# Kernel optimization log

Hardware: AMD Instinct MI355X
Metric: run time of the kernel (lower is better)

## Reference

```python
import jax, jax.numpy as jnp
import numpy as np

N, M, D = 32768, 1024, 128
TAU = 1.0  # gumbel-softmax temperature (forward default)


def setup_inputs() -> dict:
    key = jax.random.key(0)
    k1, k2, k3 = jax.random.split(key, 3)
    x = jax.random.normal(k1, (N, D), dtype=jnp.float32)
    embedding = jax.random.normal(k2, (M, D), dtype=jnp.float32)
    # torch: log_var_q_scalar initialized to log(10.0)
    log_var_q_scalar = jnp.full((1,), np.log(10.0), dtype=jnp.float32)
    # uniform noise for gumbel-softmax (replaces torch.rand_like)
    u = jax.random.uniform(k3, (N, M), dtype=jnp.float32)
    return {"x": x, "embedding": embedding,
            "log_var_q_scalar": log_var_q_scalar, "u": u}


def reference(x, embedding, log_var_q_scalar, u):
    # gaussian_1: a single scalar precision shared by all tokens/dims, so the
    # precision-weighted squared distance factorizes; expand ||x-e||^2 via a
    # GEMM instead of materializing the (N, M, D) broadcast tensor.
    precision = jnp.exp(-log_var_q_scalar)[0]                 # scalar
    x2 = jnp.sum(x * x, axis=-1, keepdims=True)               # (N, 1)
    e2 = jnp.sum(embedding * embedding, axis=-1)              # (M,)
    xe = x @ embedding.T                                      # (N, M)
    distances = 0.5 * precision * (x2 - 2.0 * xe + e2)        # (N, M)

    indices = jnp.argmin(distances, axis=-1)                  # (N,) int
    logits = -distances

    # gumbel-softmax (soft)
    eps = jnp.finfo(logits.dtype).eps
    gumbels = -jnp.log(-jnp.log(jnp.clip(u, eps, 1.0 - eps)))
    encodings = jax.nn.softmax((logits + gumbels) / TAU, axis=-1)  # (N, M)
    quantized = encodings @ embedding                              # (N, D)

    log_probs = jax.nn.log_softmax(logits, axis=-1)
    probs = jnp.exp(log_probs)
    # torch.mean over a 0-d result == the scalar itself
    loss = 0.5 * precision * jnp.sum((x - quantized) ** 2) \
           + jnp.sum(probs * log_probs)

    one_hot = jax.nn.one_hot(indices, embedding.shape[0], dtype=jnp.float32)
    avg_probs = jnp.mean(one_hot, axis=0)
    perplexity = jnp.exp(-jnp.sum(avg_probs * jnp.log(avg_probs + 1e-10)))
    return quantized, indices, loss, perplexity
```

## Files before the change

kernel.cpp:

```cpp
#include <hip/hip_runtime.h>
#include <math.h>

#define N_TOK 32768
#define M_EMB 1024
#define D_DIM 128

#define WS_EH  0
#define WS_EL  262144
#define WS_PVG 524288
#define WS_E2  1048576
#define WS_CNT (WS_E2 + 4096)
#define WS_SS  (WS_CNT + 4096)
#define WS_ENT (WS_SS + 4)
#define WS_DONE (WS_ENT + 4)

typedef float  f32x4  __attribute__((ext_vector_type(4)));
typedef short  s16x8  __attribute__((ext_vector_type(8)));
typedef short  s16x4  __attribute__((ext_vector_type(4)));
typedef __bf16 bf16x8 __attribute__((ext_vector_type(8)));

__device__ __forceinline__ ushort f2bf(float f) {
    unsigned x = __float_as_uint(f);
    unsigned r = (x + 0x7fffu + ((x >> 16) & 1u)) >> 16;
    return (ushort)r;
}
__device__ __forceinline__ float bf2f(ushort h) {
    return __uint_as_float(((unsigned)h) << 16);
}
__device__ __forceinline__ f32x4 mfma_k32(s16x8 a, s16x8 b, f32x4 c) {
    return __builtin_amdgcn_mfma_f32_16x16x32_bf16(
        __builtin_bit_cast(bf16x8, a), __builtin_bit_cast(bf16x8, b), c, 0, 0, 0);
}
__device__ __forceinline__ f32x4 mfma_k16(s16x4 a, s16x4 b, f32x4 c) {
#if __has_builtin(__builtin_amdgcn_mfma_f32_16x16x16bf16_1k)
    return __builtin_amdgcn_mfma_f32_16x16x16bf16_1k(a, b, c, 0, 0, 0);
#else
    asm("v_mfma_f32_16x16x16_bf16 %0, %1, %2, %0" : "+v"(c) : "v"(a), "v"(b));
    return c;
#endif
}
__device__ __forceinline__ void gl_lds16(const void* g, void* l) {
    __builtin_amdgcn_global_load_lds(
        (const __attribute__((address_space(1))) unsigned int*)g,
        (__attribute__((address_space(3))) unsigned int*)l, 16, 0, 0);
}

__global__ void k_prep(const float* __restrict__ emb, char* ws) {
    __shared__ ushort th_s[16][128];
    __shared__ ushort tl_s[16][128];
    if (blockIdx.x == 0) {
        int* cnt = (int*)(ws + WS_CNT);
        for (int i = threadIdx.x; i < M_EMB; i += 256) cnt[i] = 0;
        if (threadIdx.x == 0) {
            *(float*)(ws + WS_SS) = 0.f;
            *(float*)(ws + WS_ENT) = 0.f;
            *(int*)(ws + WS_DONE) = 0;
        }
    }
    ushort* eh = (ushort*)(ws + WS_EH);
    ushort* el = (ushort*)(ws + WS_EL);
    ushort* pvg = (ushort*)(ws + WS_PVG);
    float* e2 = (float*)(ws + WS_E2);
    const int m0 = blockIdx.x * 16;
    const int t = threadIdx.x;
    #pragma unroll
    for (int ii = 0; ii < 8; ii++) {
        int idx = t + ii * 256;
        int mi = idx >> 7, k = idx & 127;
        float v = emb[(size_t)(m0 + mi) * D_DIM + k];
        ushort hi = f2bf(v);
        ushort lo = f2bf(v - bf2f(hi));
        eh[(size_t)(m0 + mi) * D_DIM + k] = hi;
        el[(size_t)(m0 + mi) * D_DIM + k] = lo;
        th_s[mi][k] = hi;
        tl_s[mi][k] = lo;
    }
    __syncthreads();
    {
        const int d = t >> 1;
        const int gl2 = t & 1;
        #pragma unroll
        for (int gg = 0; gg < 2; gg++) {
            const int gl = gl2 * 2 + gg;
            s16x8 vv;
            #pragma unroll
            for (int kk = 0; kk < 4; kk++) {
                vv[kk]     = (short)th_s[gl * 4 + kk][d];
                vv[4 + kk] = (short)tl_s[gl * 4 + kk][d];
            }
            *(s16x8*)(pvg + (size_t)d * 2048 + ((m0 >> 2) + gl) * 8) = vv;
        }
    }
    if (t < 16) {
        float s = 0.f;
        const float* er = emb + (size_t)(m0 + t) * D_DIM;
        #pragma unroll 4
        for (int k = 0; k < 128; k++) s += er[k] * er[k];
        e2[m0 + t] = s;
    }
}

__global__ __launch_bounds__(256, 2) void k_main(
    const float* __restrict__ x, const float* __restrict__ emb,
    const float* __restrict__ lvq, const float* __restrict__ u,
    float* __restrict__ out, char* __restrict__ ws)
{
    __shared__ __align__(16) ushort qkh[2][32 * 128];
    __shared__ __align__(16) ushort qkl[2][32 * 128];
    __shared__ __align__(16) ushort pvt[2][128 * 64];
    __shared__ int last_flag;
    __shared__ float fin[4];

    const int t = threadIdx.x;
    const int w = t >> 6;
    const int lane = t & 63;
    const int l15 = lane & 15;
    const int h = lane >> 4;
    const int n0w = blockIdx.x * 64 + w * 16;

    const float* e2g = (const float*)(ws + WS_E2);
    int* cnt = (int*)(ws + WS_CNT);
    float* ws_ss = (float*)(ws + WS_SS);
    float* ws_ent = (float*)(ws + WS_ENT);
    const char* EHb = (const char*)(ws + WS_EH);
    const char* ELb = (const char*)(ws + WS_EL);
    const char* PVGb = (const char*)(ws + WS_PVG);

    const float prec = expf(-lvq[0]);
    const float hp = 0.5f * prec;

    int offA[8];
    if (w < 2) {
        #pragma unroll
        for (int c = 0; c < 8; c++) {
            const int s = c * 1024 + lane * 16;
            offA[c] = s ^ (((s >> 8) & 7) << 4);
        }
    } else {
        #pragma unroll
        for (int c = 0; c < 8; c++) {
            const int s = ((w - 2) * 8 + c) * 1024 + lane * 16;
            const int d = s >> 7;
            offA[c] = d * 4096 + ((s ^ ((d & 7) << 4)) & 127);
        }
    }

    s16x8 xh[4], xl[4];
    {
        const float* xr = x + (size_t)(n0w + l15) * D_DIM;
        #pragma unroll
        for (int ks = 0; ks < 4; ks++) {
            const int k0 = ks * 32 + h * 8;
            float4 v0 = *(const float4*)(xr + k0);
            float4 v1 = *(const float4*)(xr + k0 + 4);
            float vv[8] = {v0.x, v0.y, v0.z, v0.w, v1.x, v1.y, v1.z, v1.w};
            s16x8 hi8, lo8;
            #pragma unroll
            for (int j = 0; j < 8; j++) {
                ushort hi = f2bf(vv[j]);
                hi8[j] = (short)hi;
                lo8[j] = (short)f2bf(vv[j] - bf2f(hi));
            }
            xh[ks] = hi8;
            xl[ks] = lo8;
        }
    }

    const f32x4 zz = {0.f, 0.f, 0.f, 0.f};
    f32x4 qacc[8];
    #pragma unroll
    for (int dt = 0; dt < 8; dt++) qacc[dt] = zz;

    float S = 0.f, T = 0.f, Sg = 0.f;
    float bv1 = -INFINITY, bv2 = -INFINITY;
    int bi1 = M_EMB, bi2 = M_EMB;

    const float* urow = u + (size_t)(n0w + l15) * M_EMB;
    const float EPS = 1.1920929e-07f, OME = 0.99999988f;

    #define STAGE(MB, B)                                                      \
        do {                                                                  \
            if (w == 0) {                                                     \
                const char* src_ = EHb + (size_t)(MB) * 256;                  \
                _Pragma("unroll")                                             \
                for (int c_ = 0; c_ < 8; c_++)                                \
                    gl_lds16(src_ + offA[c_], &qkh[B][c_ * 512]);             \
            } else if (w == 1) {                                              \
                const char* src_ = ELb + (size_t)(MB) * 256;                  \
                _Pragma("unroll")                                             \
                for (int c_ = 0; c_ < 8; c_++)                                \
                    gl_lds16(src_ + offA[c_], &qkl[B][c_ * 512]);             \
            } else {                                                          \
                const char* src_ = PVGb + (size_t)(MB) * 4;                   \
                _Pragma("unroll")                                             \
                for (int c_ = 0; c_ < 8; c_++)                                \
                    gl_lds16(src_ + offA[c_],                                 \
                             &pvt[B][((w - 2) * 8 + c_) * 512]);              \
            }                                                                 \
        } while (0)

    STAGE(0, 0);
    __syncthreads();

    int cur = 0;
    const int Mq = (l15 & 7) << 4;

    #pragma unroll 1
    for (int mc = 0; mc < 32; mc++) {
        const int mb = mc * 32;
        float4 uvv[2];
        #pragma unroll
        for (int t2 = 0; t2 < 2; t2++)
            uvv[t2] = *(const float4*)(urow + mb + t2 * 16 + h * 4);
        if (mc < 31) {
            if (cur) STAGE(mb + 32, 0); else STAGE(mb + 32, 1);
        }

        #pragma unroll
        for (int t2 = 0; t2 < 2; t2++) {
            const int msub = mb + t2 * 16;
            const int r = t2 * 16 + l15;
            const char* qhB = (const char*)qkh[cur] + r * 256;
            const char* qlB = (const char*)qkl[cur] + r * 256;
            f32x4 aa = zz, ab = zz, ac = zz;
            #pragma unroll
            for (int ks = 0; ks < 4; ks++) {
                const int cb = (h * 16 + ks * 64) ^ Mq;
                const s16x8 ah = *(const s16x8*)(qhB + cb);
                const s16x8 al = *(const s16x8*)(qlB + cb);
                aa = mfma_k32(ah, xh[ks], aa);
                ab = mfma_k32(al, xh[ks], ab);
                ac = mfma_k32(ah, xl[ks], ac);
            }
            const float4 e2v = *(const float4*)(e2g + msub + h * 4);
            const float uu[4] = {uvv[t2].x, uvv[t2].y, uvv[t2].z, uvv[t2].w};
            const float ee[4] = {e2v.x, e2v.y, e2v.z, e2v.w};
            ushort pb[4];
            #pragma unroll
            for (int j = 0; j < 4; j++) {
                const int m = msub + h * 4 + j;
                const float v = prec * (aa[j] + ab[j] + ac[j]) - hp * ee[j];
                if (v > bv1) {
                    bv2 = bv1; bi2 = bi1;
                    bv1 = v; bi1 = m;
                } else if (v > bv2) {
                    bv2 = v; bi2 = m;
                }
                const float e = __expf(v);
                S += e; T += e * v;
                const float uc = fminf(fmaxf(uu[j], EPS), OME);
                const float d1 = 1.0f - uc;
                const float Lser = d1 * (1.0f + d1 * (0.5f + d1 * (0.33333334f + d1 * 0.25f)));
                const float Lnat = -__logf(uc);
                const float L = (d1 < 0.03125f) ? Lser : Lnat;
                const float pt = e * __builtin_amdgcn_rcpf(L);
                Sg += pt;
                pb[j] = f2bf(pt);
            }
            s16x4 pa;
            pa[0] = (short)pb[0]; pa[1] = (short)pb[1];
            pa[2] = (short)pb[2]; pa[3] = (short)pb[3];
            const char* pvB = (const char*)pvt[cur]
                            + ((l15 * 128 + (t2 * 4 + h) * 16) ^ Mq);
            #pragma unroll
            for (int dt = 0; dt < 8; dt++) {
                const s16x8 pv2 = *(const s16x8*)(pvB + dt * 2048);
                const s16x4 bh = __builtin_shufflevector(pv2, pv2, 0, 1, 2, 3);
                const s16x4 bl = __builtin_shufflevector(pv2, pv2, 4, 5, 6, 7);
                qacc[dt] = mfma_k16(pa, bh, qacc[dt]);
                qacc[dt] = mfma_k16(pa, bl, qacc[dt]);
            }
        }
        __syncthreads();
        cur ^= 1;
    }
    #undef STAGE

    #pragma unroll
    for (int off = 16; off <= 32; off <<= 1) {
        S += __shfl_xor(S, off);
        T += __shfl_xor(T, off);
        Sg += __shfl_xor(Sg, off);
        const float ov1 = __shfl_xor(bv1, off); const int oi1 = __shfl_xor(bi1, off);
        const float ov2 = __shfl_xor(bv2, off); const int oi2 = __shfl_xor(bi2, off);
        if (ov1 > bv1 || (ov1 == bv1 && oi1 < bi1)) {
            if (bv1 > ov2 || (bv1 == ov2 && bi1 < oi2)) { bv2 = bv1; bi2 = bi1; }
            else { bv2 = ov2; bi2 = oi2; }
            bv1 = ov1; bi1 = oi1;
        } else if (ov1 > bv2 || (ov1 == bv2 && oi1 < bi2)) {
            bv2 = ov1; bi2 = oi1;
        }
    }
    float inv[4];
    #pragma unroll
    for (int j = 0; j < 4; j++)
        inv[j] = 1.0f / __shfl(Sg, 4 * h + j);

    {
        float ent = T / S - __logf(S);
        #pragma unroll
        for (int off = 1; off <= 8; off <<= 1) ent += __shfl_xor(ent, off);
        if (lane == 0) atomicAdd(ws_ent, ent);
    }

    {
        const float* xr = x + (size_t)(n0w + l15) * D_DIM + h * 32;
        const float* ea = emb + (size_t)bi1 * D_DIM + h * 32;
        const float* eb = emb + (size_t)bi2 * D_DIM + h * 32;
        float s1 = 0.f, s2 = 0.f;
        #pragma unroll
        for (int i = 0; i < 8; i++) {
            const float4 xv = ((const float4*)xr)[i];
            const float4 av = ((const float4*)ea)[i];
            const float4 bb = ((const float4*)eb)[i];
            s1 += xv.x * av.x + xv.y * av.y + xv.z * av.z + xv.w * av.w;
            s2 += xv.x * bb.x + xv.y * bb.y + xv.z * bb.z + xv.w * bb.w;
        }
        #pragma unroll
        for (int off = 16; off <= 32; off <<= 1) {
            s1 += __shfl_xor(s1, off);
            s2 += __shfl_xor(s2, off);
        }
        const float g1 = prec * s1 - hp * e2g[bi1];
        const float g2 = prec * s2 - hp * e2g[bi2];
        const int win = (g2 > g1 || (g2 == g1 && bi2 < bi1)) ? bi2 : bi1;
        if (lane < 16) {
            out[(size_t)N_TOK * D_DIM + n0w + lane] = (float)win;
            atomicAdd(&cnt[win], 1);
        }
    }

    float ssl = 0.f;
    #pragma unroll
    for (int dt = 0; dt < 8; dt++) {
        #pragma unroll
        for (int j = 0; j < 4; j++) {
            const int n = n0w + 4 * h + j;
            const int d = dt * 16 + l15;
            const float q = qacc[dt][j] * inv[j];
            out[(size_t)n * D_DIM + d] = q;
            const float df = x[(size_t)n * D_DIM + d] - q;
            ssl += df * df;
        }
    }
    #pragma unroll
    for (int off = 1; off <= 32; off <<= 1) ssl += __shfl_xor(ssl, off);
    if (lane == 0) atomicAdd(ws_ss, ssl);

    __syncthreads();
    if (t == 0) {
        const int prev = __hip_atomic_fetch_add((int*)(ws + WS_DONE), 1,
                            __ATOMIC_ACQ_REL, __HIP_MEMORY_SCOPE_AGENT);
        last_flag = (prev == (int)gridDim.x - 1);
    }
    __syncthreads();
    if (last_flag) {
        float s = 0.f;
        for (int i = t; i < M_EMB; i += 256) {
            const int c = __hip_atomic_load(&cnt[i], __ATOMIC_RELAXED,
                                            __HIP_MEMORY_SCOPE_AGENT);
            const float avg = (float)c * (1.f / N_TOK);
            s += avg * logf(avg + 1e-10f);
        }
        #pragma unroll
        for (int off = 32; off >= 1; off >>= 1) s += __shfl_down(s, off);
        if ((t & 63) == 0) fin[t >> 6] = s;
        __syncthreads();
        if (t == 0) {
            const float tot = fin[0] + fin[1] + fin[2] + fin[3];
            const float perp = expf(-tot);
            const float ssv = __hip_atomic_load(ws_ss, __ATOMIC_RELAXED,
                                                __HIP_MEMORY_SCOPE_AGENT);
            const float env = __hip_atomic_load(ws_ent, __ATOMIC_RELAXED,
                                                __HIP_MEMORY_SCOPE_AGENT);
            out[(size_t)N_TOK * D_DIM + N_TOK] = hp * ssv + env;
            out[(size_t)N_TOK * D_DIM + N_TOK + 1] = perp;
        }
    }
}

extern "C" void kernel_launch(void* const* d_in, const int* in_sizes, int n_in,
                              void* d_out, int out_size, void* d_ws, size_t ws_size,
                              hipStream_t stream) {
    const float* x   = (const float*)d_in[0];
    const float* emb = (const float*)d_in[1];
    const float* lvq = (const float*)d_in[2];
    const float* u   = (const float*)d_in[3];
    float* out = (float*)d_out;
    char* ws = (char*)d_ws;
    k_prep<<<dim3(M_EMB / 16), dim3(256), 0, stream>>>(emb, ws);
    k_main<<<dim3(N_TOK / 64), dim3(256), 0, stream>>>(x, emb, lvq, u, out, ws);
}
```

Baseline: 334.8 us.

## Split codebook range across wave pairs with 512-thread blocks and cross-wave merge

Each 64-token block now launches 512 threads, and every pair of waves shares 16 tokens. One wave of the pair handles the first half of the codebook and the other the second half. Each half-set of four waves stages its own tiles into its own LDS buffer. Softmax sums, top-2 argmin candidates and the quantized accumulators are merged through shared memory at the end. The aim is more waves per CU and a shorter serial loop per wave, at the cost of losing the double-buffered prefetch (now two barriers per step) and of extra merge traffic.

```diff
diff --git a/kernel.cpp b/kernel.cpp
--- a/kernel.cpp
+++ b/kernel.cpp
@@ -100,23 +100,26 @@
     }
 }
 
-__global__ __launch_bounds__(256, 2) void k_main(
+__global__ __launch_bounds__(512, 4) void k_main(
     const float* __restrict__ x, const float* __restrict__ emb,
     const float* __restrict__ lvq, const float* __restrict__ u,
     float* __restrict__ out, char* __restrict__ ws)
 {
-    __shared__ __align__(16) ushort qkh[2][32 * 128];
-    __shared__ __align__(16) ushort qkl[2][32 * 128];
-    __shared__ __align__(16) ushort pvt[2][128 * 64];
-    __shared__ int last_flag;
-    __shared__ float fin[4];
+    __shared__ __align__(16) ushort qkh2[2][32 * 128];
+    __shared__ __align__(16) ushort qkl2[2][32 * 128];
+    __shared__ __align__(16) ushort pvt2[2][128 * 64];
+    float* sf = (float*)pvt2;
 
     const int t = threadIdx.x;
     const int w = t >> 6;
     const int lane = t & 63;
     const int l15 = lane & 15;
     const int h = lane >> 4;
-    const int n0w = blockIdx.x * 64 + w * 16;
+    const int p = w >> 1;
+    const int q = w & 1;
+    const int rw = w & 3;
+    const int sset = w >> 2;
+    const int n0p = blockIdx.x * 64 + p * 16;
 
     const float* e2g = (const float*)(ws + WS_E2);
     int* cnt = (int*)(ws + WS_CNT);
@@ -130,24 +133,24 @@
     const float hp = 0.5f * prec;
 
     int offA[8];
-    if (w < 2) {
+    if (rw < 2) {
         #pragma unroll
         for (int c = 0; c < 8; c++) {
-            const int s = c * 1024 + lane * 16;
-            offA[c] = s ^ (((s >> 8) & 7) << 4);
+            const int s_ = c * 1024 + lane * 16;
+            offA[c] = s_ ^ (((s_ >> 8) & 7) << 4);
         }
     } else {
         #pragma unroll
         for (int c = 0; c < 8; c++) {
-            const int s = ((w - 2) * 8 + c) * 1024 + lane * 16;
-            const int d = s >> 7;
-            offA[c] = d * 4096 + ((s ^ ((d & 7) << 4)) & 127);
+            const int s_ = ((rw - 2) * 8 + c) * 1024 + lane * 16;
+            const int d_ = s_ >> 7;
+            offA[c] = d_ * 4096 + ((s_ ^ ((d_ & 7) << 4)) & 127);
         }
     }
 
     s16x8 xh[4], xl[4];
     {
-        const float* xr = x + (size_t)(n0w + l15) * D_DIM;
+        const float* xr = x + (size_t)(n0p + l15) * D_DIM;
         #pragma unroll
         for (int ks = 0; ks < 4; ks++) {
             const int k0 = ks * 32 + h * 8;
@@ -175,53 +178,51 @@
     float bv1 = -INFINITY, bv2 = -INFINITY;
     int bi1 = M_EMB, bi2 = M_EMB;
 
-    const float* urow = u + (size_t)(n0w + l15) * M_EMB;
+    const float* urow = u + (size_t)(n0p + l15) * M_EMB;
     const float EPS = 1.1920929e-07f, OME = 0.99999988f;
 
-    #define STAGE(MB, B)                                                      \
+    #define STAGE(S_)                                                         \
         do {                                                                  \
-            if (w == 0) {                                                     \
-                const char* src_ = EHb + (size_t)(MB) * 256;                  \
+            const int MB_ = ((sset << 4) + (S_)) << 5;                        \
+            if (rw == 0) {                                                    \
+                const char* src_ = EHb + (size_t)MB_ * 256;                   \
                 _Pragma("unroll")                                             \
                 for (int c_ = 0; c_ < 8; c_++)                                \
-                    gl_lds16(src_ + offA[c_], &qkh[B][c_ * 512]);             \
-            } else if (w == 1) {                                              \
-                const char* src_ = ELb + (size_t)(MB) * 256;                  \
+                    gl_lds16(src_ + offA[c_], &qkh2[sset][c_ * 512]);         \
+            } else if (rw == 1) {                                             \
+                const char* src_ = ELb + (size_t)MB_ * 256;                   \
                 _Pragma("unroll")                                             \
                 for (int c_ = 0; c_ < 8; c_++)                                \
-                    gl_lds16(src_ + offA[c_], &qkl[B][c_ * 512]);             \
+                    gl_lds16(src_ + offA[c_], &qkl2[sset][c_ * 512]);         \
             } else {                                                          \
-                const char* src_ = PVGb + (size_t)(MB) * 4;                   \
+                const char* src_ = PVGb + (size_t)MB_ * 4;                    \
                 _Pragma("unroll")                                             \
                 for (int c_ = 0; c_ < 8; c_++)                                \
                     gl_lds16(src_ + offA[c_],                                 \
-                             &pvt[B][((w - 2) * 8 + c_) * 512]);              \
+                             &pvt2[sset][((rw - 2) * 8 + c_) * 512]);         \
             }                                                                 \
         } while (0)
 
-    STAGE(0, 0);
-    __syncthreads();
-
-    int cur = 0;
     const int Mq = (l15 & 7) << 4;
 
     #pragma unroll 1
-    for (int mc = 0; mc < 32; mc++) {
+    for (int s = 0; s < 16; s++) {
+        const int mc = q * 16 + s;
         const int mb = mc * 32;
         float4 uvv[2];
         #pragma unroll
         for (int t2 = 0; t2 < 2; t2++)
             uvv[t2] = *(const float4*)(urow + mb + t2 * 16 + h * 4);
-        if (mc < 31) {
-            if (cur) STAGE(mb + 32, 0); else STAGE(mb + 32, 1);
-        }
+        __syncthreads();
+        STAGE(s);
+        __syncthreads();
 
         #pragma unroll
         for (int t2 = 0; t2 < 2; t2++) {
             const int msub = mb + t2 * 16;
             const int r = t2 * 16 + l15;
-            const char* qhB = (const char*)qkh[cur] + r * 256;
-            const char* qlB = (const char*)qkl[cur] + r * 256;
+            const char* qhB = (const char*)qkh2[q] + r * 256;
+            const char* qlB = (const char*)qkl2[q] + r * 256;
             f32x4 aa = zz, ab = zz, ac = zz;
             #pragma unroll
             for (int ks = 0; ks < 4; ks++) {
@@ -260,7 +261,7 @@
             s16x4 pa;
             pa[0] = (short)pb[0]; pa[1] = (short)pb[1];
             pa[2] = (short)pb[2]; pa[3] = (short)pb[3];
-            const char* pvB = (const char*)pvt[cur]
+            const char* pvB = (const char*)pvt2[q]
                             + ((l15 * 128 + (t2 * 4 + h) * 16) ^ Mq);
             #pragma unroll
             for (int dt = 0; dt < 8; dt++) {
@@ -271,8 +272,6 @@
                 qacc[dt] = mfma_k16(pa, bl, qacc[dt]);
             }
         }
-        __syncthreads();
-        cur ^= 1;
     }
     #undef STAGE
 
@@ -291,20 +290,76 @@
             bv2 = ov1; bi2 = oi1;
         }
     }
+
+    __syncthreads();
+    if (lane < 16) {
+        sf[w * 16 + l15] = S;
+        sf[128 + w * 16 + l15] = T;
+        sf[256 + w * 16 + l15] = Sg;
+        sf[384 + w * 16 + l15] = bv1;
+        sf[512 + w * 16 + l15] = bv2;
+        ((int*)sf)[640 + w * 16 + l15] = bi1;
+        ((int*)sf)[768 + w * 16 + l15] = bi2;
+    }
+    __syncthreads();
+
+    {
+        const int pw = w ^ 1;
+        const float So = sf[pw * 16 + l15];
+        const float To = sf[128 + pw * 16 + l15];
+        const float Sgo = sf[256 + pw * 16 + l15];
+        const float ov1 = sf[384 + pw * 16 + l15];
+        const float ov2 = sf[512 + pw * 16 + l15];
+        const int oi1 = ((int*)sf)[640 + pw * 16 + l15];
+        const int oi2 = ((int*)sf)[768 + pw * 16 + l15];
+        S += So; T += To; Sg += Sgo;
+        if (ov1 > bv1 || (ov1 == bv1 && oi1 < bi1)) {
+            if (bv1 > ov2 || (bv1 == ov2 && bi1 < oi2)) { bv2 = bv1; bi2 = bi1; }
+            else { bv2 = ov2; bi2 = oi2; }
+            bv1 = ov1; bi1 = oi1;
+        } else if (ov1 > bv2 || (ov1 == bv2 && oi1 < bi2)) {
+            bv2 = ov1; bi2 = oi1;
+        }
+    }
     float inv[4];
     #pragma unroll
     for (int j = 0; j < 4; j++)
         inv[j] = 1.0f / __shfl(Sg, 4 * h + j);
 
-    {
+    float* qsc = (p < 2) ? ((float*)qkh2 + p * 2048)
+                         : ((float*)qkl2 + (p - 2) * 2048);
+    if (q == 1) {
+        #pragma unroll
+        for (int dt = 0; dt < 8; dt++)
+            #pragma unroll
+            for (int j = 0; j < 4; j++)
+                qsc[(dt * 4 + j) * 64 + lane] = qacc[dt][j];
+    }
+    __syncthreads();
+
+    if (q == 0) {
+        float ssl = 0.f;
+        #pragma unroll
+        for (int dt = 0; dt < 8; dt++) {
+            #pragma unroll
+            for (int j = 0; j < 4; j++) {
+                const float qv = (qacc[dt][j] + qsc[(dt * 4 + j) * 64 + lane]) * inv[j];
+                const int n = n0p + 4 * h + j;
+                const int d = dt * 16 + l15;
+                out[(size_t)n * D_DIM + d] = qv;
+                const float df = x[(size_t)n * D_DIM + d] - qv;
+                ssl += df * df;
+            }
+        }
+        #pragma unroll
+        for (int off = 1; off <= 32; off <<= 1) ssl += __shfl_xor(ssl, off);
+        if (lane == 0) atomicAdd(ws_ss, ssl);
+    } else {
         float ent = T / S - __logf(S);
         #pragma unroll
         for (int off = 1; off <= 8; off <<= 1) ent += __shfl_xor(ent, off);
         if (lane == 0) atomicAdd(ws_ent, ent);
-    }
-
-    {
-        const float* xr = x + (size_t)(n0w + l15) * D_DIM + h * 32;
+        const float* xr = x + (size_t)(n0p + l15) * D_DIM + h * 32;
         const float* ea = emb + (size_t)bi1 * D_DIM + h * 32;
         const float* eb = emb + (size_t)bi2 * D_DIM + h * 32;
         float s1 = 0.f, s2 = 0.f;
@@ -325,38 +380,23 @@
         const float g2 = prec * s2 - hp * e2g[bi2];
         const int win = (g2 > g1 || (g2 == g1 && bi2 < bi1)) ? bi2 : bi1;
         if (lane < 16) {
-            out[(size_t)N_TOK * D_DIM + n0w + lane] = (float)win;
+            out[(size_t)N_TOK * D_DIM + n0p + lane] = (float)win;
             atomicAdd(&cnt[win], 1);
         }
     }
 
-    float ssl = 0.f;
-    #pragma unroll
-    for (int dt = 0; dt < 8; dt++) {
-        #pragma unroll
-        for (int j = 0; j < 4; j++) {
-            const int n = n0w + 4 * h + j;
-            const int d = dt * 16 + l15;
-            const float q = qacc[dt][j] * inv[j];
-            out[(size_t)n * D_DIM + d] = q;
-            const float df = x[(size_t)n * D_DIM + d] - q;
-            ssl += df * df;
-        }
-    }
-    #pragma unroll
-    for (int off = 1; off <= 32; off <<= 1) ssl += __shfl_xor(ssl, off);
-    if (lane == 0) atomicAdd(ws_ss, ssl);
-
-    __syncthreads();
+    __syncthreads();
+    int* lf = (int*)(sf + 904);
+    float* fin = sf + 896;
     if (t == 0) {
         const int prev = __hip_atomic_fetch_add((int*)(ws + WS_DONE), 1,
                             __ATOMIC_ACQ_REL, __HIP_MEMORY_SCOPE_AGENT);
-        last_flag = (prev == (int)gridDim.x - 1);
-    }
-    __syncthreads();
-    if (last_flag) {
+        *lf = (prev == (int)gridDim.x - 1);
+    }
+    __syncthreads();
+    if (*lf) {
         float s = 0.f;
-        for (int i = t; i < M_EMB; i += 256) {
+        for (int i = t; i < M_EMB; i += 512) {
             const int c = __hip_atomic_load(&cnt[i], __ATOMIC_RELAXED,
                                             __HIP_MEMORY_SCOPE_AGENT);
             const float avg = (float)c * (1.f / N_TOK);
@@ -367,7 +407,9 @@
         if ((t & 63) == 0) fin[t >> 6] = s;
         __syncthreads();
         if (t == 0) {
-            const float tot = fin[0] + fin[1] + fin[2] + fin[3];
+            float tot = 0.f;
+            #pragma unroll
+            for (int i = 0; i < 8; i++) tot += fin[i];
             const float perp = expf(-tot);
             const float ssv = __hip_atomic_load(ws_ss, __ATOMIC_RELAXED,
                                                 __HIP_MEMORY_SCOPE_AGENT);
@@ -389,5 +431,5 @@
     float* out = (float*)d_out;
     char* ws = (char*)d_ws;
     k_prep<<<dim3(M_EMB / 16), dim3(256), 0, stream>>>(emb, ws);
-    k_main<<<dim3(N_TOK / 64), dim3(256), 0, stream>>>(x, emb, lvq, u, out, ws);
-}
+    k_main<<<dim3(N_TOK / 64), dim3(512), 0, stream>>>(x, emb, lvq, u, out, ws);
+}
```

Measured after the change: 398.6 us. 19.1% more time.
